# Optimization experiments

Hardware: AMD Instinct MI355X
Metric: run time of the kernel (lower is better)

## Reference

```python
import jax, jax.numpy as jnp
import numpy as np

B, P = 4, 2048
N = B * P
QD = 512            # query_dim == inner_dim (pos_emb is added to raw features)
CD = 512            # context_dim
HEADS, DH = 8, 64
INNER = HEADS * DH
SCALE = DH ** -0.5
HC, WC = 32, 32     # context spatial grid
L = HC * WC         # context_len
SELF_HW = 512       # spatial_dim[:2]
STRIDE = 8          # resolution_level == sparse tensor stride
PE_H = SELF_HW // STRIDE  # 64 BEV pos-emb grid


def setup_inputs() -> dict:
    key = jax.random.key(0)
    k = jax.random.split(key, 9)
    return {
        "feats": jax.random.normal(k[0], (N, QD), jnp.float32),
        "coords_xy": jax.random.randint(k[1], (N, 2), 0, SELF_HW),
        "context_emb": jax.random.normal(k[2], (B, HC, WC, CD), jnp.float32),
        "Wq": jax.random.normal(k[3], (QD, INNER), jnp.float32) * 0.02,
        "Wk": jax.random.normal(k[4], (CD, INNER), jnp.float32) * 0.02,
        "Wv": jax.random.normal(k[5], (CD, INNER), jnp.float32) * 0.02,
        "Wo": jax.random.normal(k[6], (INNER, QD), jnp.float32) * 0.02,
        "bo": jnp.zeros((QD,), jnp.float32),
        "pos_embedding": jax.random.normal(k[7], (PE_H, PE_H, INNER), jnp.float32) / INNER ** 0.5,
        "context_pos_embedding": jax.random.normal(k[8], (L, CD), jnp.float32) / INNER ** 0.5,
    }


def _neighbor_mask(coords_xy):
    # get_context_mask: scatter a (2*STRIDE+1)^2 neighborhood around each point's
    # projected context cell into a [N, L] boolean mask
    ratio = jnp.float32(HC) / jnp.float32(SELF_HW)
    center = jnp.round(coords_xy.astype(jnp.float32) * ratio).astype(jnp.int32)  # [N,2]
    off = jnp.stack(
        jnp.meshgrid(jnp.arange(-STRIDE, STRIDE + 1), jnp.arange(-STRIDE, STRIDE + 1), indexing="ij"),
        axis=-1,
    ).reshape(-1, 2)  # [K,2], K = 289
    pos = center[:, None, :] + off[None, :, :]        # [N,K,2]
    r = jnp.clip(pos[..., 0], 0, HC - 1)
    c = jnp.clip(pos[..., 1], 0, WC - 1)
    flat = r * WC + c                                  # [N,K]
    return jnp.zeros((N, L), jnp.bool_).at[jnp.arange(N)[:, None], flat].set(True)


def reference(feats, coords_xy, context_emb, Wq, Wk, Wv, Wo, bo, pos_embedding, context_pos_embedding):
    # get_context: add learned context positional embedding, flatten spatial -> [B, L, CD]
    ctx = (context_emb + context_pos_embedding.reshape(HC, WC, CD)).reshape(B, L, CD)
    # get_pos_emb: gather BEV positional embedding per point via floor(coord/stride)
    rc = coords_xy // STRIDE                           # [N,2] in [0, 64)
    pe = pos_embedding[rc[:, 0], rc[:, 1]]             # [N, INNER]
    f = (feats + pe).reshape(B, P, QD)                 # points grouped per batch (equal counts)
    mask = _neighbor_mask(coords_xy).reshape(B, P, L)
    q = (f @ Wq).reshape(B, P, HEADS, DH).transpose(0, 2, 1, 3)    # [B,h,P,d]
    k = (ctx @ Wk).reshape(B, L, HEADS, DH).transpose(0, 2, 1, 3)  # [B,h,L,d]
    v = (ctx @ Wv).reshape(B, L, HEADS, DH).transpose(0, 2, 1, 3)
    sim = jnp.einsum("bhid,bhjd->bhij", q, k) * SCALE              # [B,h,P,L]
    neg = -jnp.finfo(sim.dtype).max
    sim = jnp.where(mask[:, None, :, :], sim, neg)
    attn = jax.nn.softmax(sim, axis=-1)
    out = jnp.einsum("bhij,bhjd->bhid", attn, v)
    out = out.transpose(0, 2, 1, 3).reshape(B, P, INNER)
    out = out @ Wo + bo                                # to_out (dropout=0, eval)
    return out.reshape(N, QD)                          # scatter back to point features
```

## Files before the change

### kernel.cpp

```cpp
#include <hip/hip_runtime.h>


typedef __attribute__((ext_vector_type(8))) short bf16x8;
typedef __attribute__((ext_vector_type(4))) float f32x4;

#define SCL 0.18033688f

__device__ __forceinline__ unsigned short f2bf(float x) {
  union { float f; unsigned int u; } v; v.f = x;
  unsigned int r = v.u + 0x7FFFu + ((v.u >> 16) & 1u);
  return (unsigned short)(r >> 16);
}

__device__ __forceinline__ unsigned int pk2bf(float a, float b) {
  return (unsigned)f2bf(a) | ((unsigned)f2bf(b) << 16);
}

__device__ __forceinline__ unsigned int cvtpk(float a, float b) {
  unsigned int r;
  asm("v_cvt_pk_bf16_f32 %0, %1, %2" : "=v"(r) : "v"(a), "v"(b));
  return r;
}

__device__ __forceinline__ float fexp2(float x) {
#if __has_builtin(__builtin_amdgcn_exp2f)
  return __builtin_amdgcn_exp2f(x);
#else
  return exp2f(x);
#endif
}

__device__ __forceinline__ void gload16(const unsigned short* g, char* l) {
  __builtin_amdgcn_global_load_lds(
      (const __attribute__((address_space(1))) unsigned int*)g,
      (__attribute__((address_space(3))) unsigned int*)l, 16, 0, 0);
}

__device__ __forceinline__ int swzb(int row, int chk) {
  return row * 128 + ((chk * 16) ^ ((row & 7) << 4));
}
__device__ __forceinline__ int swz32(int row, int chk) {
  return row * 64 + ((chk << 4) ^ ((row & 3) << 4));
}

__global__ __launch_bounds__(256) void prep_all(const float* __restrict__ Wq, const float* __restrict__ Wk,
                                                const float* __restrict__ Wv, const float* __restrict__ Wo,
                                                const float* __restrict__ feats,
                                                const int* __restrict__ coords,
                                                const float* __restrict__ pos_emb,
                                                const float* __restrict__ ctx,
                                                const float* __restrict__ ctx_pos,
                                                unsigned short* __restrict__ Wqt, unsigned short* __restrict__ Wkt,
                                                unsigned short* __restrict__ Wvt, unsigned short* __restrict__ Wot,
                                                unsigned short* __restrict__ Aq,
                                                unsigned short* __restrict__ Ac,
                                                int* __restrict__ perm) {
  const int bid = blockIdx.x;
  const int t = threadIdx.x;
  if (bid < 256) {
    __shared__ float tile[64][65];
    const int wsel = bid >> 6, tt = bid & 63;
    const int kt = (tt >> 3) << 6, ntb = (tt & 7) << 6;
    const float* W = (wsel == 0) ? Wq : (wsel == 1) ? Wk : (wsel == 2) ? Wv : Wo;
    unsigned short* Wt = (wsel == 0) ? Wqt : (wsel == 1) ? Wkt : (wsel == 2) ? Wvt : Wot;
#pragma unroll
    for (int p = 0; p < 16; ++p) {
      int e = p * 256 + t;
      int row = e >> 6, col = e & 63;
      tile[row][col] = W[(long)(kt + row) * 512 + ntb + col];
    }
    __syncthreads();
#pragma unroll
    for (int p = 0; p < 16; ++p) {
      int e = p * 256 + t;
      int n = e >> 6, k = e & 63;
      Wt[(long)(ntb + n) * 512 + kt + k] = f2bf(tile[k][n]);
    }
    return;
  }
  if (bid >= 6400) {
    __shared__ int hist[64];
    __shared__ int base[64];
    const int bb = bid - 6400;
    if (t < 64) hist[t] = 0;
    __syncthreads();
    int keys[8];
#pragma unroll
    for (int i = 0; i < 8; ++i) {
      int q = bb * 2048 + t * 8 + i;
      int cr = (int)rintf((float)coords[2 * q] * 0.0625f);
      keys[i] = cr;
      atomicAdd(&hist[cr], 1);
    }
    __syncthreads();
    if (t == 0) {
      int s = 0;
      for (int k2 = 0; k2 < 64; ++k2) { base[k2] = s; s += hist[k2]; }
    }
    __syncthreads();
#pragma unroll
    for (int i = 0; i < 8; ++i) {
      int pos = atomicAdd(&base[keys[i]], 1);
      perm[bb * 2048 + pos] = t * 8 + i;
    }
    return;
  }
  int i = (bid - 256) * 256 + t;
  if (i < 1048576) {
    int e = i << 2;
    int q = e >> 9, k = e & 511;
    int pi = ((coords[2 * q] >> 3) << 6) + (coords[2 * q + 1] >> 3);
    float4 a = *(const float4*)(feats + e);
    float4 p = *(const float4*)(pos_emb + ((size_t)pi << 9) + k);
    uint2 o;
    o.x = pk2bf(a.x + p.x, a.y + p.y);
    o.y = pk2bf(a.z + p.z, a.w + p.w);
    *(uint2*)(Aq + e) = o;
  } else {
    int e = (i - 1048576) << 2;
    int r = e >> 9, k = e & 511;
    float4 a = *(const float4*)(ctx + e);
    float4 p = *(const float4*)(ctx_pos + ((size_t)(r & 1023) << 9) + k);
    uint2 o;
    o.x = pk2bf(a.x + p.x, a.y + p.y);
    o.y = pk2bf(a.z + p.z, a.w + p.w);
    *(uint2*)(Ac + e) = o;
  }
}

__global__ __launch_bounds__(256) void gemm_qkv(const unsigned short* __restrict__ Aq,
                                                const unsigned short* __restrict__ Ac,
                                                const unsigned short* __restrict__ Wqt,
                                                const unsigned short* __restrict__ Wkt,
                                                const unsigned short* __restrict__ Wvt,
                                                unsigned short* __restrict__ Qb,
                                                unsigned short* __restrict__ Kb,
                                                unsigned short* __restrict__ Vt) {
  __shared__ char Asf[2][8192];
  __shared__ char Bsf[2][8192];
  const int t = threadIdx.x, l = t & 63, wv = t >> 6;
  const int wr = (wv >> 1) << 6, wc = (wv & 1) << 6;
  const int orig = blockIdx.x;
  const int bx = (orig & 7) * 64 + (orig >> 3);
  const bool isQ = bx < 256;
  long tm; const unsigned short* Bt; const unsigned short* Ab; bool isV = false; int nt;
  if (isQ) {
    tm = (long)(bx >> 2) * 128;
    nt = bx & 3;
    Bt = Wqt + (long)nt * 65536;
    Ab = Aq;
  } else {
    const int kvx = bx - 256;
    tm = (long)(kvx >> 3) * 128;
    const int y = kvx & 7;
    isV = y >= 4; nt = y & 3;
    Bt = (isV ? Wvt : Wkt) + (long)nt * 65536;
    Ab = Ac;
  }

  auto STAGE = [&](int buf, int k0) {
#pragma unroll
    for (int i = 0; i < 2; ++i) {
      int row = i * 64 + wv * 16 + (l >> 2);
      int chs = (l & 3) ^ (row & 3);
      char* dst = &(Asf[buf][i * 4096 + wv * 1024]);
      gload16(Ab + (tm + row) * 512 + k0 + chs * 8, dst);
      char* dstB = &(Bsf[buf][i * 4096 + wv * 1024]);
      gload16(Bt + (long)row * 512 + k0 + chs * 8, dstB);
    }
  };

  STAGE(0, 0);
  __syncthreads();

  f32x4 acc[4][4] = {};
  const int lr = l & 15, g = l >> 4;

  for (int s = 0; s < 16; ++s) {
    const int cur = s & 1;
    if (s < 15) STAGE(cur ^ 1, (s + 1) << 5);
    bf16x8 af[4], bfr[4];
#pragma unroll
    for (int i = 0; i < 4; ++i) {
      af[i]  = *(const bf16x8*)(Asf[cur] + swz32(wr + i * 16 + lr, g));
      bfr[i] = *(const bf16x8*)(Bsf[cur] + swz32(wc + i * 16 + lr, g));
    }
#pragma unroll
    for (int mi = 0; mi < 4; ++mi)
#pragma unroll
      for (int ni = 0; ni < 4; ++ni)
        acc[mi][ni] = __builtin_amdgcn_mfma_f32_16x16x32_bf16(af[mi], bfr[ni], acc[mi][ni], 0, 0, 0);
    __syncthreads();
  }

  const int lq = g << 2;
#pragma unroll
  for (int mi = 0; mi < 4; ++mi)
#pragma unroll
    for (int ni = 0; ni < 4; ++ni) {
      int cn = nt * 128 + wc + ni * 16 + lr;
      long r0 = tm + wr + mi * 16 + lq;
      if (isQ) {
#pragma unroll
        for (int r = 0; r < 4; ++r)
          Qb[(r0 + r) * 512 + cn] = f2bf(acc[mi][ni][r] * SCL);
      } else if (!isV) {
#pragma unroll
        for (int r = 0; r < 4; ++r)
          Kb[(r0 + r) * 512 + cn] = f2bf(acc[mi][ni][r]);
      } else {
        int h = cn >> 6, d = cn & 63;
#pragma unroll
        for (int r = 0; r < 4; ++r) {
          long row = r0 + r;
          int b = (int)(row >> 10), j = (int)(row & 1023);
          int jp = (j & ~63) | ((j & 15) << 2) | ((j >> 4) & 3);
          Vt[((long)(b * 8 + h) * 64 + d) * 1024 + jp] = f2bf(acc[mi][ni][r]);
        }
      }
    }
}

__global__ __launch_bounds__(512, 4) void attn_mfma(const unsigned short* __restrict__ Qb,
                                                    const unsigned short* __restrict__ Kb,
                                                    const unsigned short* __restrict__ Vt,
                                                    const int* __restrict__ coords,
                                                    const int* __restrict__ perm,
                                                    unsigned short* __restrict__ Abf) {
  __shared__ char Kl[2][8192];
  __shared__ char Vl[2][8192];
  __shared__ char Ol[2048];
  __shared__ unsigned short Plds[8][16][72];
  __shared__ int permL[128];
  __shared__ int rng[2];
  const int t = threadIdx.x, w = t >> 6, l = t & 63;
  const int g = l >> 4, lc = l & 15;
  const int orig = blockIdx.x;
  const int sw = (orig & 7) * 64 + (orig >> 3);
  const int qx = sw & 15, bh = sw >> 4;
  const int b = bh >> 3, h = bh & 7;

  if (t < 128) permL[t] = perm[b * 2048 + qx * 128 + t];
  if (t == 0) { rng[0] = 63; rng[1] = 0; }
  __syncthreads();

  int rm[4], cm[4];
  int lrmin = 63, lrmax = 0;
#pragma unroll
  for (int r = 0; r < 4; ++r) {
    long qq = (long)b * 2048 + permL[w * 16 + g * 4 + r];
    int cr = (int)rintf((float)coords[2 * qq] * 0.0625f);
    int cc = (int)rintf((float)coords[2 * qq + 1] * 0.0625f);
    int rlo = max(0, cr - 8), rhi = min(31, cr + 8);
    int clo = max(0, cc - 8), chi = min(31, cc + 8);
    rm[r] = (int)((((unsigned)1 << (rhi - rlo + 1)) - 1) << rlo);
    cm[r] = (int)((((unsigned)1 << (chi - clo + 1)) - 1) << clo);
    lrmin = min(lrmin, rlo); lrmax = max(lrmax, rhi);
  }
#pragma unroll
  for (int off = 32; off > 0; off >>= 1) {
    lrmin = min(lrmin, __shfl_xor(lrmin, off));
    lrmax = max(lrmax, __shfl_xor(lrmax, off));
  }
  const int wt0 = lrmin >> 1, wt1 = lrmax >> 1;
  if (l == 0) { atomicMin(&rng[0], lrmin); atomicMax(&rng[1], lrmax); }

  bf16x8 qfr[2];
  {
    long qrow = (long)b * 2048 + permL[w * 16 + lc];
#pragma unroll
    for (int dc = 0; dc < 2; ++dc)
      qfr[dc] = *(const bf16x8*)(Qb + qrow * 512 + h * 64 + dc * 32 + g * 8);
  }

  const unsigned short* Kg = Kb + ((long)b * 1024) * 512 + h * 64;
  const unsigned short* Vg = Vt + ((long)bh * 64) * 1024;

  const int srow = t >> 3;
  const int chs = (l & 7) ^ ((l >> 3) & 7);
  auto STAGE = [&](int buf, int kt_) {
    const int kb_ = kt_ * 64;
    gload16(Kg + (long)(kb_ + srow) * 512 + chs * 8, Kl[buf] + w * 1024);
    gload16(Vg + (long)srow * 1024 + kb_ + chs * 8, Vl[buf] + w * 1024);
  };

  if (t < 128) {
    int r = t >> 3, c = t & 7;
    unsigned short vv = (r == 0) ? (unsigned short)0x3F80 : (unsigned short)0;
    unsigned short tmp[8] = {vv, vv, vv, vv, vv, vv, vv, vv};
    *(int4*)(Ol + swzb(r, c)) = *(int4*)tmp;
  }
  __syncthreads();
  const int t0 = rng[0] >> 1, t1 = rng[1] >> 1;
  STAGE(0, t0);
  __syncthreads();

  f32x4 po[5] = {};

  for (int kt = t0; kt <= t1; ++kt) {
    const int cur = (kt - t0) & 1;
    const int kb = kt * 64;
    if (kt < t1) STAGE(cur ^ 1, kt + 1);

    if (kt >= wt0 && kt <= wt1) {
      bf16x8 kfr[4][2];
#pragma unroll
      for (int kf = 0; kf < 4; ++kf)
#pragma unroll
        for (int dc = 0; dc < 2; ++dc)
          kfr[kf][dc] = *(const bf16x8*)(Kl[cur] + swzb(kf * 16 + lc, dc * 4 + g));

      f32x4 sv[4];
      __builtin_amdgcn_s_setprio(1);
#pragma unroll
      for (int kf = 0; kf < 4; ++kf) {
        f32x4 a = {};
        a = __builtin_amdgcn_mfma_f32_16x16x32_bf16(qfr[0], kfr[kf][0], a, 0, 0, 0);
        a = __builtin_amdgcn_mfma_f32_16x16x32_bf16(qfr[1], kfr[kf][1], a, 0, 0, 0);
        sv[kf] = a;
      }
      __builtin_amdgcn_s_setprio(0);

      const int jrb = kb >> 5;
      int cmk[4][4];
#pragma unroll
      for (int kf = 0; kf < 4; ++kf) {
        int jr = jrb + (kf >> 1);
#pragma unroll
        for (int r = 0; r < 4; ++r)
          cmk[kf][r] = ((rm[r] >> jr) & 1) ? cm[r] : 0;
      }
#pragma unroll
      for (int kf = 0; kf < 4; ++kf) {
        int jc = ((kf & 1) << 4) + lc;
#pragma unroll
        for (int r = 0; r < 4; ++r) {
          float p = fexp2(sv[kf][r]);
          sv[kf][r] = ((cmk[kf][r] >> jc) & 1) ? p : 0.0f;
        }
      }

      bf16x8 vfr[5][2];
#pragma unroll
      for (int df = 0; df < 4; ++df)
#pragma unroll
        for (int kc = 0; kc < 2; ++kc)
          vfr[df][kc] = *(const bf16x8*)(Vl[cur] + swzb(df * 16 + lc, kc * 4 + g));
#pragma unroll
      for (int kc = 0; kc < 2; ++kc)
        vfr[4][kc] = *(const bf16x8*)(Ol + swzb(lc, kc * 4 + g));

#pragma unroll
      for (int r = 0; r < 4; ++r) {
        uint2 pk;
        pk.x = cvtpk(sv[0][r], sv[1][r]);
        pk.y = cvtpk(sv[2][r], sv[3][r]);
        *(uint2*)(&Plds[w][g * 4 + r][4 * lc]) = pk;
      }

      bf16x8 pa0 = *(const bf16x8*)(&Plds[w][lc][g * 8]);
      bf16x8 pa1 = *(const bf16x8*)(&Plds[w][lc][32 + g * 8]);
      __builtin_amdgcn_s_setprio(1);
#pragma unroll
      for (int df = 0; df < 5; ++df) {
        po[df] = __builtin_amdgcn_mfma_f32_16x16x32_bf16(pa0, vfr[df][0], po[df], 0, 0, 0);
        po[df] = __builtin_amdgcn_mfma_f32_16x16x32_bf16(pa1, vfr[df][1], po[df], 0, 0, 0);
      }
      __builtin_amdgcn_s_setprio(0);
    }

    __syncthreads();
  }

#pragma unroll
  for (int r = 0; r < 4; ++r) {
    float lsum = __shfl(po[4][r], l & 48);
    float inv = 1.0f / lsum;
    long qr = (long)b * 2048 + permL[w * 16 + g * 4 + r];
#pragma unroll
    for (int df = 0; df < 4; ++df)
      Abf[qr * 512 + h * 64 + df * 16 + lc] = f2bf(po[df][r] * inv);
  }
}

__global__ __launch_bounds__(256) void gemm_o(const unsigned short* __restrict__ A,
                                              const unsigned short* __restrict__ Bt,
                                              float* __restrict__ C,
                                              const float* __restrict__ bias) {
  __shared__ char Asf[2][4096];
  __shared__ char Bsf[2][8192];
  const int t = threadIdx.x, l = t & 63, wv = t >> 6;
  const int wr = (wv >> 1) << 5;
  const int wc = (wv & 1) << 6;
  const int orig = blockIdx.x;
  const int bx = (orig & 7) * 64 + (orig >> 3);
  const long tm = (long)(bx >> 2) * 64;
  const long tn = (long)(bx & 3) * 128;

  auto STAGE = [&](int buf, int k0) {
    {
      int row = wv * 16 + (l >> 2);
      int chs = (l & 3) ^ (row & 3);
      char* dst = &(Asf[buf][wv * 1024]);
      gload16(A + (tm + row) * 512 + k0 + chs * 8, dst);
    }
#pragma unroll
    for (int i = 0; i < 2; ++i) {
      int row = i * 64 + wv * 16 + (l >> 2);
      int chs = (l & 3) ^ (row & 3);
      char* dst = &(Bsf[buf][i * 4096 + wv * 1024]);
      gload16(Bt + (tn + row) * 512 + k0 + chs * 8, dst);
    }
  };

  STAGE(0, 0);
  __syncthreads();

  f32x4 acc[2][4] = {};
  const int lr = l & 15, g = l >> 4;

  for (int s = 0; s < 16; ++s) {
    const int cur = s & 1;
    if (s < 15) STAGE(cur ^ 1, (s + 1) << 5);
    bf16x8 af[2], bfr[4];
#pragma unroll
    for (int i = 0; i < 2; ++i)
      af[i] = *(const bf16x8*)(Asf[cur] + swz32(wr + i * 16 + lr, g));
#pragma unroll
    for (int i = 0; i < 4; ++i)
      bfr[i] = *(const bf16x8*)(Bsf[cur] + swz32(wc + i * 16 + lr, g));
#pragma unroll
    for (int mi = 0; mi < 2; ++mi)
#pragma unroll
      for (int ni = 0; ni < 4; ++ni)
        acc[mi][ni] = __builtin_amdgcn_mfma_f32_16x16x32_bf16(af[mi], bfr[ni], acc[mi][ni], 0, 0, 0);
    __syncthreads();
  }

  const int lq = g << 2;
#pragma unroll
  for (int mi = 0; mi < 2; ++mi)
#pragma unroll
    for (int ni = 0; ni < 4; ++ni) {
      long col = tn + wc + ni * 16 + lr;
      float bv = bias[col];
      long r0 = tm + wr + mi * 16 + lq;
#pragma unroll
      for (int r = 0; r < 4; ++r)
        C[(r0 + r) * 512 + col] = acc[mi][ni][r] + bv;
    }
}

extern "C" void kernel_launch(void* const* d_in, const int* in_sizes, int n_in,
                              void* d_out, int out_size, void* d_ws, size_t ws_size,
                              hipStream_t stream) {
  (void)in_sizes; (void)n_in; (void)out_size; (void)ws_size;
  const float* feats   = (const float*)d_in[0];
  const int*   coords  = (const int*)d_in[1];
  const float* ctx     = (const float*)d_in[2];
  const float* Wq      = (const float*)d_in[3];
  const float* Wk      = (const float*)d_in[4];
  const float* Wv      = (const float*)d_in[5];
  const float* Wo      = (const float*)d_in[6];
  const float* bo      = (const float*)d_in[7];
  const float* pos_emb = (const float*)d_in[8];
  const float* ctx_pos = (const float*)d_in[9];
  float* out = (float*)d_out;
  char* ws = (char*)d_ws;

  unsigned short* Wqt = (unsigned short*)(ws);
  unsigned short* Wkt = (unsigned short*)(ws + 524288);
  unsigned short* Wvt = (unsigned short*)(ws + 1048576);
  unsigned short* Wot = (unsigned short*)(ws + 1572864);
  unsigned short* Aq  = (unsigned short*)(ws + 2097152);
  unsigned short* Ac  = (unsigned short*)(ws + 10485760);
  unsigned short* Qb  = (unsigned short*)(ws + 14680064);
  unsigned short* Kb  = (unsigned short*)(ws + 23068672);
  unsigned short* Vt  = (unsigned short*)(ws + 27262976);
  unsigned short* Abf = (unsigned short*)(ws + 31457280);
  int*            prm = (int*)(ws + 39845888);

  prep_all<<<6404, 256, 0, stream>>>(Wq, Wk, Wv, Wo, feats, coords, pos_emb, ctx, ctx_pos,
                                     Wqt, Wkt, Wvt, Wot, Aq, Ac, prm);
  gemm_qkv<<<512, 256, 0, stream>>>(Aq, Ac, Wqt, Wkt, Wvt, Qb, Kb, Vt);
  attn_mfma<<<512, 512, 0, stream>>>(Qb, Kb, Vt, coords, prm, Abf);
  gemm_o  <<<512, 256, 0, stream>>>(Abf, Wot, out, bo);
}
```

Before: 80.44 us.

## Deepen K prefetch to quad-buffered ring with partial vmcnt waits

```diff
diff --git a/kernel.cpp b/kernel.cpp
--- a/kernel.cpp
+++ b/kernel.cpp
@@ -227,7 +227,7 @@
                                                     const int* __restrict__ coords,
                                                     const int* __restrict__ perm,
                                                     unsigned short* __restrict__ Abf) {
-  __shared__ char Kl[2][8192];
+  __shared__ char Kl[4][8192];
   __shared__ char Vl[2][8192];
   __shared__ char Ol[2048];
   __shared__ unsigned short Plds[8][16][72];
@@ -278,10 +278,11 @@
 
   const int srow = t >> 3;
   const int chs = (l & 7) ^ ((l >> 3) & 7);
-  auto STAGE = [&](int buf, int kt_) {
-    const int kb_ = kt_ * 64;
-    gload16(Kg + (long)(kb_ + srow) * 512 + chs * 8, Kl[buf] + w * 1024);
-    gload16(Vg + (long)srow * 1024 + kb_ + chs * 8, Vl[buf] + w * 1024);
+  auto STAGEK = [&](int buf, int kt_) {
+    gload16(Kg + (long)(kt_ * 64 + srow) * 512 + chs * 8, Kl[buf] + w * 1024);
+  };
+  auto STAGEV = [&](int buf, int kt_) {
+    gload16(Vg + (long)srow * 1024 + kt_ * 64 + chs * 8, Vl[buf] + w * 1024);
   };
 
   if (t < 128) {
@@ -292,15 +293,20 @@
   }
   __syncthreads();
   const int t0 = rng[0] >> 1, t1 = rng[1] >> 1;
-  STAGE(0, t0);
-  __syncthreads();
+  STAGEV(0, t0);
+  STAGEK(0, t0);
+  STAGEK(1, min(t0 + 1, t1));
+  asm volatile("s_waitcnt vmcnt(1)" ::: "memory");
+  __builtin_amdgcn_s_barrier();
+  __builtin_amdgcn_sched_barrier(0);
 
   f32x4 po[5] = {};
 
   for (int kt = t0; kt <= t1; ++kt) {
-    const int cur = (kt - t0) & 1;
-    const int kb = kt * 64;
-    if (kt < t1) STAGE(cur ^ 1, kt + 1);
+    const int i = kt - t0;
+    const int curK = i & 3, curV = i & 1;
+    STAGEV(curV ^ 1, min(kt + 1, t1));
+    STAGEK((i + 2) & 3, min(kt + 2, t1));
 
     if (kt >= wt0 && kt <= wt1) {
       bf16x8 kfr[4][2];
@@ -308,7 +314,7 @@
       for (int kf = 0; kf < 4; ++kf)
 #pragma unroll
         for (int dc = 0; dc < 2; ++dc)
-          kfr[kf][dc] = *(const bf16x8*)(Kl[cur] + swzb(kf * 16 + lc, dc * 4 + g));
+          kfr[kf][dc] = *(const bf16x8*)(Kl[curK] + swzb(kf * 16 + lc, dc * 4 + g));
 
       f32x4 sv[4];
       __builtin_amdgcn_s_setprio(1);
@@ -321,7 +327,7 @@
       }
       __builtin_amdgcn_s_setprio(0);
 
-      const int jrb = kb >> 5;
+      const int jrb = (kt * 64) >> 5;
       int cmk[4][4];
 #pragma unroll
       for (int kf = 0; kf < 4; ++kf) {
@@ -345,7 +351,7 @@
       for (int df = 0; df < 4; ++df)
 #pragma unroll
         for (int kc = 0; kc < 2; ++kc)
-          vfr[df][kc] = *(const bf16x8*)(Vl[cur] + swzb(df * 16 + lc, kc * 4 + g));
+          vfr[df][kc] = *(const bf16x8*)(Vl[curV] + swzb(df * 16 + lc, kc * 4 + g));
 #pragma unroll
       for (int kc = 0; kc < 2; ++kc)
         vfr[4][kc] = *(const bf16x8*)(Ol + swzb(lc, kc * 4 + g));
@@ -369,7 +375,9 @@
       __builtin_amdgcn_s_setprio(0);
     }
 
-    __syncthreads();
+    asm volatile("s_waitcnt vmcnt(1)" ::: "memory");
+    __builtin_amdgcn_s_barrier();
+    __builtin_amdgcn_sched_barrier(0);
   }
 
 #pragma unroll
```

Result: no change. 80.85 us (+0.5%).

## Process two query fragments per wave in attention to reuse K/V tile loads

Applied to the files above, without the earlier changes.

```diff
diff --git a/kernel.cpp b/kernel.cpp
--- a/kernel.cpp
+++ b/kernel.cpp
@@ -221,16 +221,15 @@
     }
 }
 
-__global__ __launch_bounds__(512, 4) void attn_mfma(const unsigned short* __restrict__ Qb,
-                                                    const unsigned short* __restrict__ Kb,
-                                                    const unsigned short* __restrict__ Vt,
-                                                    const int* __restrict__ coords,
-                                                    const int* __restrict__ perm,
-                                                    unsigned short* __restrict__ Abf) {
+__global__ __launch_bounds__(256) void attn_mfma(const unsigned short* __restrict__ Qb,
+                                                 const unsigned short* __restrict__ Kb,
+                                                 const unsigned short* __restrict__ Vt,
+                                                 const int* __restrict__ coords,
+                                                 const int* __restrict__ perm,
+                                                 unsigned short* __restrict__ Abf) {
   __shared__ char Kl[2][8192];
   __shared__ char Vl[2][8192];
-  __shared__ char Ol[2048];
-  __shared__ unsigned short Plds[8][16][72];
+  __shared__ unsigned short Plds[4][32][72];
   __shared__ int permL[128];
   __shared__ int rng[2];
   const int t = threadIdx.x, w = t >> 6, l = t & 63;
@@ -244,19 +243,21 @@
   if (t == 0) { rng[0] = 63; rng[1] = 0; }
   __syncthreads();
 
-  int rm[4], cm[4];
+  int rm[8], cm[8];
   int lrmin = 63, lrmax = 0;
 #pragma unroll
-  for (int r = 0; r < 4; ++r) {
-    long qq = (long)b * 2048 + permL[w * 16 + g * 4 + r];
-    int cr = (int)rintf((float)coords[2 * qq] * 0.0625f);
-    int cc = (int)rintf((float)coords[2 * qq + 1] * 0.0625f);
-    int rlo = max(0, cr - 8), rhi = min(31, cr + 8);
-    int clo = max(0, cc - 8), chi = min(31, cc + 8);
-    rm[r] = (int)((((unsigned)1 << (rhi - rlo + 1)) - 1) << rlo);
-    cm[r] = (int)((((unsigned)1 << (chi - clo + 1)) - 1) << clo);
-    lrmin = min(lrmin, rlo); lrmax = max(lrmax, rhi);
-  }
+  for (int qf = 0; qf < 2; ++qf)
+#pragma unroll
+    for (int r = 0; r < 4; ++r) {
+      long qq = (long)b * 2048 + permL[w * 32 + qf * 16 + g * 4 + r];
+      int cr = (int)rintf((float)coords[2 * qq] * 0.0625f);
+      int cc = (int)rintf((float)coords[2 * qq + 1] * 0.0625f);
+      int rlo = max(0, cr - 8), rhi = min(31, cr + 8);
+      int clo = max(0, cc - 8), chi = min(31, cc + 8);
+      rm[qf * 4 + r] = (int)((((unsigned)1 << (rhi - rlo + 1)) - 1) << rlo);
+      cm[qf * 4 + r] = (int)((((unsigned)1 << (chi - clo + 1)) - 1) << clo);
+      lrmin = min(lrmin, rlo); lrmax = max(lrmax, rhi);
+    }
 #pragma unroll
   for (int off = 32; off > 0; off >>= 1) {
     lrmin = min(lrmin, __shfl_xor(lrmin, off));
@@ -265,41 +266,42 @@
   const int wt0 = lrmin >> 1, wt1 = lrmax >> 1;
   if (l == 0) { atomicMin(&rng[0], lrmin); atomicMax(&rng[1], lrmax); }
 
-  bf16x8 qfr[2];
-  {
-    long qrow = (long)b * 2048 + permL[w * 16 + lc];
+  bf16x8 qfr[2][2];
+#pragma unroll
+  for (int qf = 0; qf < 2; ++qf) {
+    long qrow = (long)b * 2048 + permL[w * 32 + qf * 16 + lc];
 #pragma unroll
     for (int dc = 0; dc < 2; ++dc)
-      qfr[dc] = *(const bf16x8*)(Qb + qrow * 512 + h * 64 + dc * 32 + g * 8);
+      qfr[qf][dc] = *(const bf16x8*)(Qb + qrow * 512 + h * 64 + dc * 32 + g * 8);
   }
 
   const unsigned short* Kg = Kb + ((long)b * 1024) * 512 + h * 64;
   const unsigned short* Vg = Vt + ((long)bh * 64) * 1024;
 
-  const int srow = t >> 3;
   const int chs = (l & 7) ^ ((l >> 3) & 7);
   auto STAGE = [&](int buf, int kt_) {
-    const int kb_ = kt_ * 64;
-    gload16(Kg + (long)(kb_ + srow) * 512 + chs * 8, Kl[buf] + w * 1024);
-    gload16(Vg + (long)srow * 1024 + kb_ + chs * 8, Vl[buf] + w * 1024);
+#pragma unroll
+    for (int i = 0; i < 2; ++i) {
+      int row = i * 32 + w * 8 + (l >> 3);
+      gload16(Kg + (long)(kt_ * 64 + row) * 512 + chs * 8, Kl[buf] + i * 4096 + w * 1024);
+      gload16(Vg + (long)row * 1024 + kt_ * 64 + chs * 8, Vl[buf] + i * 4096 + w * 1024);
+    }
   };
 
-  if (t < 128) {
-    int r = t >> 3, c = t & 7;
-    unsigned short vv = (r == 0) ? (unsigned short)0x3F80 : (unsigned short)0;
-    unsigned short tmp[8] = {vv, vv, vv, vv, vv, vv, vv, vv};
-    *(int4*)(Ol + swzb(r, c)) = *(int4*)tmp;
-  }
+  const unsigned short ov = (lc == 0) ? (unsigned short)0x3F80 : (unsigned short)0;
+  bf16x8 onesf;
+#pragma unroll
+  for (int i = 0; i < 8; ++i) onesf[i] = (short)ov;
+
   __syncthreads();
   const int t0 = rng[0] >> 1, t1 = rng[1] >> 1;
   STAGE(0, t0);
   __syncthreads();
 
-  f32x4 po[5] = {};
+  f32x4 po[2][5] = {};
 
   for (int kt = t0; kt <= t1; ++kt) {
     const int cur = (kt - t0) & 1;
-    const int kb = kt * 64;
     if (kt < t1) STAGE(cur ^ 1, kt + 1);
 
     if (kt >= wt0 && kt <= wt1) {
@@ -310,77 +312,79 @@
         for (int dc = 0; dc < 2; ++dc)
           kfr[kf][dc] = *(const bf16x8*)(Kl[cur] + swzb(kf * 16 + lc, dc * 4 + g));
 
-      f32x4 sv[4];
+      const int jrb = kt * 2;
+#pragma unroll
+      for (int qf = 0; qf < 2; ++qf) {
+        f32x4 sv[4];
+        __builtin_amdgcn_s_setprio(1);
+#pragma unroll
+        for (int kf = 0; kf < 4; ++kf) {
+          f32x4 a = {};
+          a = __builtin_amdgcn_mfma_f32_16x16x32_bf16(qfr[qf][0], kfr[kf][0], a, 0, 0, 0);
+          a = __builtin_amdgcn_mfma_f32_16x16x32_bf16(qfr[qf][1], kfr[kf][1], a, 0, 0, 0);
+          sv[kf] = a;
+        }
+        __builtin_amdgcn_s_setprio(0);
+#pragma unroll
+        for (int kf = 0; kf < 4; ++kf) {
+          int jr = jrb + (kf >> 1);
+          int jc = ((kf & 1) << 4) + lc;
+#pragma unroll
+          for (int r = 0; r < 4; ++r) {
+            int cmask = ((rm[qf * 4 + r] >> jr) & 1) ? cm[qf * 4 + r] : 0;
+            float p = fexp2(sv[kf][r]);
+            sv[kf][r] = ((cmask >> jc) & 1) ? p : 0.0f;
+          }
+        }
+#pragma unroll
+        for (int r = 0; r < 4; ++r) {
+          uint2 pk;
+          pk.x = cvtpk(sv[0][r], sv[1][r]);
+          pk.y = cvtpk(sv[2][r], sv[3][r]);
+          *(uint2*)(&Plds[w][qf * 16 + g * 4 + r][4 * lc]) = pk;
+        }
+      }
+
+      bf16x8 pa[2][2];
+#pragma unroll
+      for (int qf = 0; qf < 2; ++qf) {
+        pa[qf][0] = *(const bf16x8*)(&Plds[w][qf * 16 + lc][g * 8]);
+        pa[qf][1] = *(const bf16x8*)(&Plds[w][qf * 16 + lc][32 + g * 8]);
+      }
+
       __builtin_amdgcn_s_setprio(1);
 #pragma unroll
-      for (int kf = 0; kf < 4; ++kf) {
-        f32x4 a = {};
-        a = __builtin_amdgcn_mfma_f32_16x16x32_bf16(qfr[0], kfr[kf][0], a, 0, 0, 0);
-        a = __builtin_amdgcn_mfma_f32_16x16x32_bf16(qfr[1], kfr[kf][1], a, 0, 0, 0);
-        sv[kf] = a;
+      for (int qf = 0; qf < 2; ++qf) {
+        po[qf][4] = __builtin_amdgcn_mfma_f32_16x16x32_bf16(pa[qf][0], onesf, po[qf][4], 0, 0, 0);
+        po[qf][4] = __builtin_amdgcn_mfma_f32_16x16x32_bf16(pa[qf][1], onesf, po[qf][4], 0, 0, 0);
+      }
+#pragma unroll
+      for (int df = 0; df < 4; ++df) {
+        bf16x8 v0 = *(const bf16x8*)(Vl[cur] + swzb(df * 16 + lc, g));
+        bf16x8 v1 = *(const bf16x8*)(Vl[cur] + swzb(df * 16 + lc, 4 + g));
+#pragma unroll
+        for (int qf = 0; qf < 2; ++qf) {
+          po[qf][df] = __builtin_amdgcn_mfma_f32_16x16x32_bf16(pa[qf][0], v0, po[qf][df], 0, 0, 0);
+          po[qf][df] = __builtin_amdgcn_mfma_f32_16x16x32_bf16(pa[qf][1], v1, po[qf][df], 0, 0, 0);
+        }
       }
       __builtin_amdgcn_s_setprio(0);
-
-      const int jrb = kb >> 5;
-      int cmk[4][4];
-#pragma unroll
-      for (int kf = 0; kf < 4; ++kf) {
-        int jr = jrb + (kf >> 1);
-#pragma unroll
-        for (int r = 0; r < 4; ++r)
-          cmk[kf][r] = ((rm[r] >> jr) & 1) ? cm[r] : 0;
-      }
-#pragma unroll
-      for (int kf = 0; kf < 4; ++kf) {
-        int jc = ((kf & 1) << 4) + lc;
-#pragma unroll
-        for (int r = 0; r < 4; ++r) {
-          float p = fexp2(sv[kf][r]);
-          sv[kf][r] = ((cmk[kf][r] >> jc) & 1) ? p : 0.0f;
-        }
-      }
-
-      bf16x8 vfr[5][2];
+    }
+
+    __syncthreads();
+  }
+
+#pragma unroll
+  for (int qf = 0; qf < 2; ++qf)
+#pragma unroll
+    for (int r = 0; r < 4; ++r) {
+      float lsum = __shfl(po[qf][4][r], l & 48);
+      float inv = 1.0f / lsum;
+      long qr = (long)b * 2048 + permL[w * 32 + qf * 16 + g * 4 + r];
 #pragma unroll
       for (int df = 0; df < 4; ++df)
-#pragma unroll
-        for (int kc = 0; kc < 2; ++kc)
-          vfr[df][kc] = *(const bf16x8*)(Vl[cur] + swzb(df * 16 + lc, kc * 4 + g));
-#pragma unroll
-      for (int kc = 0; kc < 2; ++kc)
-        vfr[4][kc] = *(const bf16x8*)(Ol + swzb(lc, kc * 4 + g));
-
-#pragma unroll
-      for (int r = 0; r < 4; ++r) {
-        uint2 pk;
-        pk.x = cvtpk(sv[0][r], sv[1][r]);
-        pk.y = cvtpk(sv[2][r], sv[3][r]);
-        *(uint2*)(&Plds[w][g * 4 + r][4 * lc]) = pk;
-      }
-
-      bf16x8 pa0 = *(const bf16x8*)(&Plds[w][lc][g * 8]);
-      bf16x8 pa1 = *(const bf16x8*)(&Plds[w][lc][32 + g * 8]);
-      __builtin_amdgcn_s_setprio(1);
-#pragma unroll
-      for (int df = 0; df < 5; ++df) {
-        po[df] = __builtin_amdgcn_mfma_f32_16x16x32_bf16(pa0, vfr[df][0], po[df], 0, 0, 0);
-        po[df] = __builtin_amdgcn_mfma_f32_16x16x32_bf16(pa1, vfr[df][1], po[df], 0, 0, 0);
-      }
-      __builtin_amdgcn_s_setprio(0);
-    }
-
-    __syncthreads();
-  }
-
-#pragma unroll
-  for (int r = 0; r < 4; ++r) {
-    float lsum = __shfl(po[4][r], l & 48);
-    float inv = 1.0f / lsum;
-    long qr = (long)b * 2048 + permL[w * 16 + g * 4 + r];
-#pragma unroll
-    for (int df = 0; df < 4; ++df)
-      Abf[qr * 512 + h * 64 + df * 16 + lc] = f2bf(po[df][r] * inv);
-  }
+        Abf[qr * 512 + h * 64 + df * 16 + lc] = f2bf(po[qf][df][r] * inv);
+    }
 }
 
 __global__ __launch_bounds__(256) void gemm_o(const unsigned short* __restrict__ A,
@@ -483,6 +487,6 @@
   prep_all<<<6404, 256, 0, stream>>>(Wq, Wk, Wv, Wo, feats, coords, pos_emb, ctx, ctx_pos,
                                      Wqt, Wkt, Wvt, Wot, Aq, Ac, prm);
   gemm_qkv<<<512, 256, 0, stream>>>(Aq, Ac, Wqt, Wkt, Wvt, Qb, Kb, Vt);
-  attn_mfma<<<512, 512, 0, stream>>>(Qb, Kb, Vt, coords, prm, Abf);
+  attn_mfma<<<512, 256, 0, stream>>>(Qb, Kb, Vt, coords, prm, Abf);
   gemm_o  <<<512, 256, 0, stream>>>(Abf, Wot, out, bo);
 }
```

After: 84.85 us. +5.5%, slower.
